# Kernel optimization log

Hardware: AMD Instinct MI355X
Metric: run time of the kernel (lower is better)

The kernel has to match this reference:

```python
import jax, jax.numpy as jnp
import numpy as np

B, N, D, H, DH, DEPTH = 4, 1024, 1024, 16, 64, 4
FI = int(D * 4.0 * 2 / 3)  # 2730, GEGLU inner dim
EPS = 1.1920929e-07  # torch float32 eps (RMSNorm default)
NEG = -jnp.finfo(jnp.float32).max


def rms(x, w):
    return x * jax.lax.rsqrt(jnp.mean(x * x, axis=-1, keepdims=True) + EPS) * w


def rope(t):
    # t: [b, h, n, d]; interleaved-pair rotary (lucidrains rotary_embedding_torch)
    n, d = t.shape[-2], t.shape[-1]
    inv_freq = 1.0 / (10000.0 ** (jnp.arange(0, d, 2, dtype=jnp.float32) / d))
    ang = jnp.arange(n, dtype=jnp.float32)[:, None] * inv_freq  # [n, d/2]
    cos = jnp.repeat(jnp.cos(ang), 2, axis=-1)  # [n, d]
    sin = jnp.repeat(jnp.sin(ang), 2, axis=-1)
    x = t.reshape(t.shape[:-1] + (d // 2, 2))
    rot = jnp.stack([-x[..., 1], x[..., 0]], axis=-1).reshape(t.shape)
    return t * cos + rot * sin


def setup_inputs() -> dict:
    key = jax.random.key(0)
    ks = jax.random.split(key, 14)
    s = 0.02
    return {
        "x": jax.random.normal(ks[0], (B, N, D), dtype=jnp.float32),
        "norm_attn_w": jnp.ones((DEPTH, D), jnp.float32),
        "wq": jax.random.normal(ks[1], (DEPTH, H * DH, D), jnp.float32) * s,
        "wkv": jax.random.normal(ks[2], (DEPTH, 2 * H * DH, D), jnp.float32) * s,
        "wo": jax.random.normal(ks[3], (DEPTH, D, H * DH), jnp.float32) * s,
        "wg": jax.random.normal(ks[4], (DEPTH, H, D), jnp.float32) * s,
        "wmix": jax.random.normal(ks[5], (DEPTH, H, D), jnp.float32) * s,
        "norm_ff_w": jnp.ones((DEPTH, D), jnp.float32),
        "ff_norm_w": jnp.ones((DEPTH, D), jnp.float32),
        "w_in": jax.random.normal(ks[6], (DEPTH, 2 * FI, D), jnp.float32) * s,
        "b_in": jnp.zeros((DEPTH, 2 * FI), jnp.float32),
        "w_out": jax.random.normal(ks[7], (DEPTH, D, FI), jnp.float32) * s,
        "b_out": jnp.zeros((DEPTH, D), jnp.float32),
        "final_norm_w": jnp.ones((D,), jnp.float32),
    }


def _forward(x, norm_attn_w, wq, wkv, wo, wg, wmix, norm_ff_w, ff_norm_w,
             w_in, b_in, w_out, b_out, final_norm_w):
    scale = DH ** -0.5
    causal = jnp.triu(jnp.ones((N, N), bool), k=1)  # True = masked
    value_residual = None
    for i in range(DEPTH):
        # --- attention block (pre-RMSNorm wrapper) ---
        h = rms(x, norm_attn_w[i])  # [b, n, d]
        q = jnp.einsum('bnd,ed->bne', h, wq[i]) * scale
        kv = jnp.einsum('bnd,ed->bne', h, wkv[i])
        k, v = jnp.split(kv, 2, axis=-1)
        split = lambda t: t.reshape(B, N, H, DH).transpose(0, 2, 1, 3)  # b h n d
        q, k, v = split(q), split(k), split(v)
        orig_v = v
        if value_residual is not None:
            mix = jax.nn.sigmoid(jnp.einsum('bnd,hd->bhn', h, wmix[i]))[..., None]
            v = v + mix * (value_residual - v)  # lerp(v, value_residual, mix)
        q, k = rope(q), rope(k)
        sim = jnp.einsum('bhid,bhjd->bhij', q, k)
        sim = jnp.where(causal, NEG, sim)
        attn = jax.nn.softmax(sim, axis=-1)
        out = jnp.einsum('bhij,bhjd->bhid', attn, v)
        gates = jax.nn.sigmoid(jnp.einsum('bnd,hd->bhn', h, wg[i]))[..., None]
        out = out * gates
        out = out.transpose(0, 2, 1, 3).reshape(B, N, H * DH)
        x = x + jnp.einsum('bne,de->bnd', out, wo[i])
        if value_residual is None:
            value_residual = orig_v
        # --- feedforward block (wrapper norm + FF's own pre-rmsnorm) ---
        g = rms(x, norm_ff_w[i])
        g = rms(g, ff_norm_w[i])
        u = jnp.einsum('bnd,ed->bne', g, w_in[i]) + b_in[i]
        a, gt = jnp.split(u, 2, axis=-1)
        u = a * jax.nn.gelu(gt, approximate=False)
        x = x + jnp.einsum('bnf,df->bnd', u, w_out[i]) + b_out[i]
    return rms(x, final_norm_w)


def reference(x, norm_attn_w, wq, wkv, wo, wg, wmix, norm_ff_w, ff_norm_w,
              w_in, b_in, w_out, b_out, final_norm_w):
    return _forward(x, norm_attn_w, wq, wkv, wo, wg, wmix, norm_ff_w,
                    ff_norm_w, w_in, b_in, w_out, b_out, final_norm_w)
```

## Files before the change

kernel.cpp:

```cpp
#include <hip/hip_runtime.h>
#include <cstdint>
#include <cstddef>


#define DEV_INLINE __device__ __forceinline__

typedef short bf16x8 __attribute__((ext_vector_type(8)));
typedef float f32x4 __attribute__((ext_vector_type(4)));

constexpr int Bsz = 4, Nseq = 1024, Dm = 1024, Hh = 16, DH = 64, NDEPTH = 4;
constexpr int FI = 2730;
constexpr int FI_PAD = 2752;
constexpr int FI_TILE = 2816;
constexpr int WIDE = 2 * FI_TILE;
constexpr int ROWS = Bsz * Nseq;
constexpr float EPSR = 1.1920929e-07f;

DEV_INLINE float bf2f(unsigned short u) {
  unsigned int x = ((unsigned int)u) << 16;
  float f; __builtin_memcpy(&f, &x, 4); return f;
}
DEV_INLINE unsigned short f2bf(float f) {
  unsigned int x; __builtin_memcpy(&x, &f, 4);
  unsigned int r = x + 0x7fffu + ((x >> 16) & 1u);
  return (unsigned short)(r >> 16);
}

using gptr_t = const __attribute__((address_space(1))) void*;
using lptr_t = __attribute__((address_space(3))) void*;
DEV_INLINE void gl_lds16(const void* g, void* l) {
  __builtin_amdgcn_global_load_lds((gptr_t)g, (lptr_t)l, 16, 0, 0);
}
DEV_INLINE void fence_mem() { asm volatile("" ::: "memory"); }

__global__ __launch_bounds__(256)
void convf2b(const float* __restrict__ src, unsigned short* __restrict__ dst,
             int src_rows, int src_cols, int dst_cols) {
  const int r = blockIdx.y;
  const int c8 = (blockIdx.x * blockDim.x + threadIdx.x) * 8;
  if (c8 >= dst_cols) return;
  alignas(16) unsigned short o[8];
  if (r < src_rows && c8 + 8 <= src_cols) {
    const float2* p = (const float2*)&src[(size_t)r * src_cols + c8];
    const float2 v0 = p[0], v1 = p[1], v2 = p[2], v3 = p[3];
    o[0] = f2bf(v0.x); o[1] = f2bf(v0.y); o[2] = f2bf(v1.x); o[3] = f2bf(v1.y);
    o[4] = f2bf(v2.x); o[5] = f2bf(v2.y); o[6] = f2bf(v3.x); o[7] = f2bf(v3.y);
  } else {
#pragma unroll
    for (int j = 0; j < 8; ++j) {
      const int c = c8 + j;
      float v = (r < src_rows && c < src_cols) ? src[(size_t)r * src_cols + c] : 0.0f;
      o[j] = f2bf(v);
    }
  }
  *(uint4*)&dst[(size_t)r * dst_cols + c8] = *(const uint4*)o;
}

__global__ __launch_bounds__(128)
void convf2b_g16(const float* __restrict__ src, unsigned short* __restrict__ dst) {
  const int p = blockIdx.y;
  const int c8 = threadIdx.x * 8;
  const int t = p >> 5, r5 = p & 31;
  const int srow = t * 16 + (r5 & 15);
  alignas(16) unsigned short o[8];
  if (srow < FI) {
    const size_t base = ((size_t)((r5 < 16) ? 0 : 1) * FI + srow) * 1024 + c8;
    const float4 v0 = *(const float4*)&src[base];
    const float4 v1 = *(const float4*)&src[base + 4];
    o[0]=f2bf(v0.x); o[1]=f2bf(v0.y); o[2]=f2bf(v0.z); o[3]=f2bf(v0.w);
    o[4]=f2bf(v1.x); o[5]=f2bf(v1.y); o[6]=f2bf(v1.z); o[7]=f2bf(v1.w);
  } else {
#pragma unroll
    for (int j = 0; j < 8; ++j) o[j] = 0;
  }
  *(uint4*)&dst[(size_t)p * 1024 + c8] = *(const uint4*)o;
}

__global__ __launch_bounds__(256)
void rope_tables(float* __restrict__ cost, float* __restrict__ sint) {
  int idx = blockIdx.x * 256 + threadIdx.x;
  if (idx >= Nseq * 32) return;
  int n = idx >> 5, p = idx & 31;
  float freq = powf(10000.0f, -(float)(2 * p) * (1.0f / 64.0f));
  float ang = (float)n * freq;
  cost[idx] = cosf(ang);
  sint[idx] = sinf(ang);
}

__global__ __launch_bounds__(256)
void rms_one(const float* __restrict__ x, const float* __restrict__ w,
             unsigned short* __restrict__ out) {
  __shared__ float sred[4];
  const int row = blockIdx.x, tid = threadIdx.x;
  const float4 v = ((const float4*)(x + (size_t)row * Dm))[tid];
  float ss = v.x * v.x + v.y * v.y + v.z * v.z + v.w * v.w;
#pragma unroll
  for (int o = 32; o >= 1; o >>= 1) ss += __shfl_xor(ss, o, 64);
  if ((tid & 63) == 0) sred[tid >> 6] = ss;
  __syncthreads();
  float rs = rsqrtf((sred[0] + sred[1] + sred[2] + sred[3]) * (1.0f / Dm) + EPSR);
  const float4 wv = ((const float4*)w)[tid];
  alignas(8) unsigned short o4[4] = { f2bf(v.x * rs * wv.x), f2bf(v.y * rs * wv.y),
                                      f2bf(v.z * rs * wv.z), f2bf(v.w * rs * wv.w) };
  *(uint2*)&out[(size_t)row * Dm + tid * 4] = *(const uint2*)o4;
}

__global__ __launch_bounds__(256)
void rms_ff(const float* __restrict__ x, const float* __restrict__ w1,
            const float* __restrict__ w2, unsigned short* __restrict__ out) {
  __shared__ float sred[4];
  const int row = blockIdx.x, tid = threadIdx.x;
  const float4 v = ((const float4*)(x + (size_t)row * Dm))[tid];
  const float4 w1v = ((const float4*)w1)[tid];
  const float4 w2v = ((const float4*)w2)[tid];
  float ss = v.x * v.x + v.y * v.y + v.z * v.z + v.w * v.w;
#pragma unroll
  for (int o = 32; o >= 1; o >>= 1) ss += __shfl_xor(ss, o, 64);
  if ((tid & 63) == 0) sred[tid >> 6] = ss;
  __syncthreads();
  float rs1 = rsqrtf((sred[0] + sred[1] + sred[2] + sred[3]) * (1.0f / Dm) + EPSR);
  float t0 = v.x * rs1 * w1v.x, t1 = v.y * rs1 * w1v.y;
  float t2 = v.z * rs1 * w1v.z, t3 = v.w * rs1 * w1v.w;
  float ss2 = t0 * t0 + t1 * t1 + t2 * t2 + t3 * t3;
#pragma unroll
  for (int o = 32; o >= 1; o >>= 1) ss2 += __shfl_xor(ss2, o, 64);
  __syncthreads();
  if ((tid & 63) == 0) sred[tid >> 6] = ss2;
  __syncthreads();
  float rs2 = rsqrtf((sred[0] + sred[1] + sred[2] + sred[3]) * (1.0f / Dm) + EPSR);
  alignas(8) unsigned short o4[4] = { f2bf(t0 * rs2 * w2v.x), f2bf(t1 * rs2 * w2v.y),
                                      f2bf(t2 * rs2 * w2v.z), f2bf(t3 * rs2 * w2v.w) };
  *(uint2*)&out[(size_t)row * Dm + tid * 4] = *(const uint2*)o4;
}

__global__ __launch_bounds__(256)
void rms_final(const float* __restrict__ x, const float* __restrict__ w,
               float* __restrict__ out) {
  __shared__ float sred[4];
  const int row = blockIdx.x, tid = threadIdx.x;
  const float4 v = ((const float4*)(x + (size_t)row * Dm))[tid];
  float ss = v.x * v.x + v.y * v.y + v.z * v.z + v.w * v.w;
#pragma unroll
  for (int o = 32; o >= 1; o >>= 1) ss += __shfl_xor(ss, o, 64);
  if ((tid & 63) == 0) sred[tid >> 6] = ss;
  __syncthreads();
  float rs = rsqrtf((sred[0] + sred[1] + sred[2] + sred[3]) * (1.0f / Dm) + EPSR);
  const float4 wv = ((const float4*)w)[tid];
  float4 o;
  o.x = v.x * rs * wv.x; o.y = v.y * rs * wv.y;
  o.z = v.z * rs * wv.z; o.w = v.w * rs * wv.w;
  ((float4*)(out + (size_t)row * Dm))[tid] = o;
}

template <int MODE>
__global__ __launch_bounds__(256)
void gemm_nt(const unsigned short* __restrict__ A,
             const unsigned short* __restrict__ Bw,
             void* __restrict__ Cout,
             const float* __restrict__ bias,
             const float* __restrict__ resid,
             int K, int ldc, int n_store) {
  __shared__ unsigned short As[2][128 * 64];
  __shared__ unsigned short Bs[2][128 * 64];
  const int tid = threadIdx.x;
  const int m0 = blockIdx.x * 128;
  const int n0 = blockIdx.y * 128;
  const int w = tid >> 6, l = tid & 63;
  const int wm = (w >> 1) * 64, wn = (w & 1) * 64;
  const int lr = l & 15, lg = l >> 4;
  const int lsub = l & 7, lrow8 = l >> 3;
  const int colsw = (lsub ^ lrow8) << 3;
  const unsigned short* gA = &A[(size_t)(m0 + w * 8 + lrow8) * K + colsw];
  const unsigned short* gB = &Bw[(size_t)(n0 + w * 8 + lrow8) * K + colsw];
  const size_t rstep = (size_t)32 * K;
  f32x4 acc[4][4] = {};

  auto stage = [&](int buf, int kt) {
    const int o = kt * 64;
#pragma unroll
    for (int i = 0; i < 4; ++i) {
      gl_lds16(gA + i * rstep + o, &As[buf][i * 2048 + w * 512]);
      gl_lds16(gB + i * rstep + o, &Bs[buf][i * 2048 + w * 512]);
    }
  };
  auto compute = [&](int buf) {
    bf16x8 af[2][4], bfr[2][4];
#pragma unroll
    for (int ks = 0; ks < 2; ++ks) {
      const int slot = (ks * 4 + lg) ^ (lr & 7);
#pragma unroll
      for (int fj = 0; fj < 4; ++fj)
        bfr[ks][fj] = *(const bf16x8*)&Bs[buf][(wn + fj * 16 + lr) * 64 + slot * 8];
#pragma unroll
      for (int fi = 0; fi < 4; ++fi)
        af[ks][fi] = *(const bf16x8*)&As[buf][(wm + fi * 16 + lr) * 64 + slot * 8];
    }
    __builtin_amdgcn_s_setprio(1);
#pragma unroll
    for (int ks = 0; ks < 2; ++ks)
#pragma unroll
      for (int fi = 0; fi < 4; ++fi)
#pragma unroll
        for (int fj = 0; fj < 4; ++fj)
          acc[fi][fj] = __builtin_amdgcn_mfma_f32_16x16x32_bf16(af[ks][fi], bfr[ks][fj], acc[fi][fj], 0, 0, 0);
    __builtin_amdgcn_s_setprio(0);
  };

  const int nk = K >> 6;
  stage(0, 0);
  asm volatile("s_waitcnt vmcnt(0)" ::: "memory");
  __builtin_amdgcn_s_barrier();
  fence_mem();
  int cur = 0;
#pragma unroll 1
  for (int kt = 0; kt < nk; ++kt) {
    const bool more = (kt + 1 < nk);
    if (more) stage(cur ^ 1, kt + 1);
    compute(cur);
    if (more) {
      asm volatile("s_waitcnt vmcnt(0)" ::: "memory");
      __builtin_amdgcn_s_barrier();
      fence_mem();
    }
    cur ^= 1;
  }

#pragma unroll
  for (int fi = 0; fi < 4; ++fi) {
    const int rowb = m0 + wm + fi * 16 + lg * 4;
#pragma unroll
    for (int fj = 0; fj < 4; ++fj) {
      const int col = n0 + wn + fj * 16 + lr;
#pragma unroll
      for (int r = 0; r < 4; ++r) {
        const float val = acc[fi][fj][r];
        const int rr = rowb + r;
        if constexpr (MODE == 1) {
          if (col < n_store)
            ((float*)Cout)[(size_t)rr * ldc + col] = 1.0f / (1.0f + __expf(-val));
        } else {
          const float bv = bias ? bias[col] : 0.0f;
          ((float*)Cout)[(size_t)rr * ldc + col] =
              resid[(size_t)rr * ldc + col] + val + bv;
        }
      }
    }
  }
}

template <int MODE>
__global__ __launch_bounds__(512, 2)
void gemm_nt256(const unsigned short* __restrict__ A,
                const unsigned short* __restrict__ Bw,
                void* __restrict__ Cout,
                const float* __restrict__ bias,
                int K, int ldc, int nm, int nn) {
  __shared__ unsigned short As[2][256 * 64];
  __shared__ unsigned short Bs[2][256 * 64];
  const int tid = threadIdx.x;
  const int nwg = nm * nn;
  const int qq = nwg >> 3;
  const int xcd = blockIdx.x & 7, orig = blockIdx.x >> 3;
  const int wgid = xcd * qq + orig;
  const int m0 = (wgid % nm) * 256;
  const int n0 = (wgid / nm) * 256;
  const int w = tid >> 6, l = tid & 63;
  const int wm = (w >> 2) * 128, wn = (w & 3) * 64;
  const int lr = l & 15, lg = l >> 4;
  const int lsub = l & 7, lrow8 = l >> 3;
  const int colsw = (lsub ^ lrow8) << 3;
  const unsigned short* gA = &A[(size_t)(m0 + w * 8 + lrow8) * K + colsw];
  const unsigned short* gB = &Bw[(size_t)(n0 + w * 8 + lrow8) * K + colsw];
  const size_t rstep = (size_t)64 * K;
  f32x4 acc[8][4] = {};

  auto stage_part = [&](int buf, int kt, int part) {
    const int o = kt * 64;
    const int i0 = (part & 1) * 2;
    if (part < 2) {
      gl_lds16(gA + (size_t)i0 * rstep + o,       &As[buf][i0 * 4096 + w * 512]);
      gl_lds16(gA + (size_t)(i0 + 1) * rstep + o, &As[buf][(i0 + 1) * 4096 + w * 512]);
    } else {
      gl_lds16(gB + (size_t)i0 * rstep + o,       &Bs[buf][i0 * 4096 + w * 512]);
      gl_lds16(gB + (size_t)(i0 + 1) * rstep + o, &Bs[buf][(i0 + 1) * 4096 + w * 512]);
    }
  };

  const int nk = K >> 6;
  stage_part(0, 0, 0); stage_part(0, 0, 1);
  stage_part(0, 0, 2); stage_part(0, 0, 3);
  asm volatile("s_waitcnt vmcnt(0)" ::: "memory");
  __builtin_amdgcn_s_barrier();
  fence_mem();

#pragma unroll 1
  for (int t = 0; t < nk; ++t) {
    const int p = t & 1;
    const bool more = (t + 1 < nk);
    bf16x8 bfr[4];
#pragma unroll
    for (int q = 0; q < 4; ++q) {
      const int ks = q >> 1, half = q & 1;
      const int slot = (ks * 4 + lg) ^ (lr & 7);
      if (half == 0) {
#pragma unroll
        for (int fj = 0; fj < 4; ++fj)
          bfr[fj] = *(const bf16x8*)&Bs[p][(wn + fj * 16 + lr) * 64 + slot * 8];
      }
      bf16x8 af[4];
#pragma unroll
      for (int fi = 0; fi < 4; ++fi)
        af[fi] = *(const bf16x8*)&As[p][(wm + half * 64 + fi * 16 + lr) * 64 + slot * 8];
      if (more) stage_part(p ^ 1, t + 1, q);
      __builtin_amdgcn_s_setprio(1);
#pragma unroll
      for (int fi = 0; fi < 4; ++fi)
#pragma unroll
        for (int fj = 0; fj < 4; ++fj)
          acc[half * 4 + fi][fj] =
              __builtin_amdgcn_mfma_f32_16x16x32_bf16(af[fi], bfr[fj], acc[half * 4 + fi][fj], 0, 0, 0);
      __builtin_amdgcn_s_setprio(0);
      if (q < 3) {
        __builtin_amdgcn_s_barrier();
        fence_mem();
      }
    }
    if (more) {
      asm volatile("s_waitcnt vmcnt(0)" ::: "memory");
      __builtin_amdgcn_s_barrier();
      fence_mem();
    }
  }

#pragma unroll
  for (int fi = 0; fi < 8; ++fi) {
    const int rowb = m0 + wm + fi * 16 + lg * 4;
    if constexpr (MODE == 0) {
#pragma unroll
      for (int fj = 0; fj < 4; ++fj) {
        const int col = n0 + wn + fj * 16 + lr;
#pragma unroll
        for (int r = 0; r < 4; ++r)
          ((unsigned short*)Cout)[(size_t)(rowb + r) * ldc + col] = f2bf(acc[fi][fj][r]);
      }
    } else {
#pragma unroll
      for (int fjp = 0; fjp < 2; ++fjp) {
        const int ucol = ((n0 + wn) >> 1) + fjp * 16 + lr;
        if (ucol >= FI_PAD) continue;
        const bool live = (ucol < FI);
        const float ba = live ? bias[ucol] : 0.0f;
        const float bg = live ? bias[FI + ucol] : 0.0f;
#pragma unroll
        for (int r = 0; r < 4; ++r) {
          const float va = acc[fi][2 * fjp][r] + ba;
          const float vg = acc[fi][2 * fjp + 1][r] + bg;
          const float gel = 0.5f * vg * (1.0f + erff(vg * 0.70710678118654752f));
          ((unsigned short*)Cout)[(size_t)(rowb + r) * ldc + ucol] =
              f2bf(live ? va * gel : 0.0f);
        }
      }
    }
  }
}

__global__ __launch_bounds__(256)
void rope_qk(const unsigned short* __restrict__ qkv_lin,
             const float* __restrict__ cost, const float* __restrict__ sint,
             unsigned short* __restrict__ qb, unsigned short* __restrict__ kb) {
  const int nt = blockIdx.x, bh = blockIdx.y;
  const int b = bh >> 4, h = bh & 15;
  const int tid = threadIdx.x;
  const int pi = tid & 31, r0 = tid >> 5;
  const float scale = 0.125f;
#pragma unroll
  for (int j = 0; j < 8; ++j) {
    const int n = nt * 64 + r0 + j * 8;
    const int nf = b * Nseq + n;
    const float c = cost[n * 32 + pi], s = sint[n * 32 + pi];
    const unsigned short* qp = &qkv_lin[(size_t)nf * 3072 + h * 64 + pi * 2];
    float q0 = bf2f(qp[0]), q1 = bf2f(qp[1]);
    alignas(4) unsigned short oq[2];
    oq[0] = f2bf((q0 * c - q1 * s) * scale);
    oq[1] = f2bf((q1 * c + q0 * s) * scale);
    *(unsigned int*)&qb[((size_t)bh * Nseq + n) * 64 + pi * 2] = *(const unsigned int*)oq;
    const unsigned short* kp = &qkv_lin[(size_t)nf * 3072 + 1024 + h * 64 + pi * 2];
    float k0 = bf2f(kp[0]), k1 = bf2f(kp[1]);
    alignas(4) unsigned short ok[2];
    ok[0] = f2bf(k0 * c - k1 * s);
    ok[1] = f2bf(k1 * c + k0 * s);
    *(unsigned int*)&kb[((size_t)bh * Nseq + n) * 64 + pi * 2] = *(const unsigned int*)ok;
  }
}

__global__ __launch_bounds__(256)
void v_mix_pack(const unsigned short* __restrict__ qkv_lin,
                const float* __restrict__ gm,
                unsigned short* __restrict__ vres,
                unsigned short* __restrict__ vtb, int layer) {
  __shared__ unsigned short T[64][72];
  const int nt = blockIdx.x, bh = blockIdx.y;
  const int b = bh >> 4, h = bh & 15;
  const int tid = threadIdx.x;
#pragma unroll
  for (int p = 0; p < 2; ++p) {
    int c = tid + p * 256;
    int nl = c >> 3, cg = (c & 7) << 3;
    int n = nt * 64 + nl, nf = b * Nseq + n;
    uint4 vv = *(const uint4*)&qkv_lin[(size_t)nf * 3072 + 2048 + h * 64 + cg];
    if (layer == 0) {
      *(uint4*)&vres[((size_t)bh * Nseq + n) * 64 + cg] = vv;
      *(uint4*)&T[nl][cg] = vv;
    } else {
      alignas(16) unsigned short ve[8]; *(uint4*)ve = vv;
      uint4 rv = *(const uint4*)&vres[((size_t)bh * Nseq + n) * 64 + cg];
      alignas(16) unsigned short re[8]; *(uint4*)re = rv;
      const float mix = gm[(size_t)nf * 32 + 16 + h];
      alignas(16) unsigned short oe[8];
#pragma unroll
      for (int j = 0; j < 8; ++j) {
        float v = bf2f(ve[j]), rr = bf2f(re[j]);
        oe[j] = f2bf(v + mix * (rr - v));
      }
      *(uint4*)&T[nl][cg] = *(const uint4*)oe;
    }
  }
  __syncthreads();
#pragma unroll
  for (int p = 0; p < 2; ++p) {
    int c = tid + p * 256;
    int d = c >> 3, ng = (c & 7) << 3;
    alignas(16) unsigned short oe[8];
#pragma unroll
    for (int j = 0; j < 8; ++j) oe[j] = T[ng + j][d];
    *(uint4*)&vtb[(size_t)bh * 65536 + (size_t)d * Nseq + nt * 64 + ng] = *(const uint4*)oe;
  }
}

__global__ __launch_bounds__(256)
void attn_fwd(const unsigned short* __restrict__ qb,
              const unsigned short* __restrict__ kb,
              const unsigned short* __restrict__ vtb,
              const float* __restrict__ gm,
              unsigned short* __restrict__ attn_out) {
  __shared__ unsigned short Ps[4][16][72];
  const int bid = blockIdx.x;
  const int x = bid & 7, rest = bid >> 3;
  const int bh = x * 8 + (rest & 7);
  const int qt = 15 - (rest >> 3);
  const int b = bh >> 4, h = bh & 15;
  const int tid = threadIdx.x;
  const int w = tid >> 6, l = tid & 63;
  const int lr = l & 15, lg = l >> 4;
  const int q0 = qt * 64 + w * 16;
  const size_t head = (size_t)bh * Nseq * DH;

  bf16x8 aq[2];
  aq[0] = *(const bf16x8*)&qb[head + (size_t)(q0 + lr) * DH + lg * 8];
  aq[1] = *(const bf16x8*)&qb[head + (size_t)(q0 + lr) * DH + 32 + lg * 8];

  float mrow[4] = {-1e30f, -1e30f, -1e30f, -1e30f};
  float lsum[4] = {0.f, 0.f, 0.f, 0.f};
  f32x4 acco[4] = {};

  for (int kt = 0; kt <= qt; ++kt) {
    const int kv0 = kt * 64;
    f32x4 s[4];
#pragma unroll
    for (int t = 0; t < 4; ++t) {
      bf16x8 bk0 = *(const bf16x8*)&kb[head + (size_t)(kv0 + t * 16 + lr) * DH + lg * 8];
      bf16x8 bk1 = *(const bf16x8*)&kb[head + (size_t)(kv0 + t * 16 + lr) * DH + 32 + lg * 8];
      f32x4 z = {};
      z = __builtin_amdgcn_mfma_f32_16x16x32_bf16(aq[0], bk0, z, 0, 0, 0);
      z = __builtin_amdgcn_mfma_f32_16x16x32_bf16(aq[1], bk1, z, 0, 0, 0);
      s[t] = z;
    }
    const bool diag = (kt == qt);
    float mx4[4];
    bool need = false;
#pragma unroll
    for (int r = 0; r < 4; ++r) {
      const int qr = q0 + lg * 4 + r;
      float mx = -1e30f;
#pragma unroll
      for (int t = 0; t < 4; ++t) {
        float sv = s[t][r];
        if (diag && (kv0 + t * 16 + lr > qr)) sv = -1e30f;
        s[t][r] = sv;
        mx = fmaxf(mx, sv);
      }
      mx = fmaxf(mx, __shfl_xor(mx, 1, 64));
      mx = fmaxf(mx, __shfl_xor(mx, 2, 64));
      mx = fmaxf(mx, __shfl_xor(mx, 4, 64));
      mx = fmaxf(mx, __shfl_xor(mx, 8, 64));
      mx4[r] = mx;
      need = need || (mx > mrow[r] + 8.0f);
    }
    if (__any(need)) {
#pragma unroll
      for (int r = 0; r < 4; ++r) {
        const float mn = fmaxf(mrow[r], mx4[r]);
        const float alpha = __expf(mrow[r] - mn);
        mrow[r] = mn;
        lsum[r] *= alpha;
#pragma unroll
        for (int dt = 0; dt < 4; ++dt) acco[dt][r] *= alpha;
      }
    }
#pragma unroll
    for (int r = 0; r < 4; ++r) {
      float rs = 0.f;
#pragma unroll
      for (int t = 0; t < 4; ++t) {
        float pv = __expf(s[t][r] - mrow[r]);
        s[t][r] = pv;
        rs += pv;
      }
      rs += __shfl_xor(rs, 1, 64);
      rs += __shfl_xor(rs, 2, 64);
      rs += __shfl_xor(rs, 4, 64);
      rs += __shfl_xor(rs, 8, 64);
      lsum[r] += rs;
    }
#pragma unroll
    for (int t = 0; t < 4; ++t)
#pragma unroll
      for (int r = 0; r < 4; ++r)
        Ps[w][lg * 4 + r][t * 16 + lr] = f2bf(s[t][r]);
#pragma unroll
    for (int ks = 0; ks < 2; ++ks) {
      bf16x8 ap = *(const bf16x8*)&Ps[w][lr][ks * 32 + lg * 8];
#pragma unroll
      for (int dt = 0; dt < 4; ++dt) {
        bf16x8 bv = *(const bf16x8*)&vtb[head + (size_t)(dt * 16 + lr) * Nseq + kv0 + ks * 32 + lg * 8];
        acco[dt] = __builtin_amdgcn_mfma_f32_16x16x32_bf16(ap, bv, acco[dt], 0, 0, 0);
      }
    }
  }
#pragma unroll
  for (int r = 0; r < 4; ++r) {
    const int qr = q0 + lg * 4 + r;
    const int nf = b * Nseq + qr;
    const float gate = gm[(size_t)nf * 32 + h];
    const float inv = 1.0f / lsum[r];
#pragma unroll
    for (int dt = 0; dt < 4; ++dt)
      attn_out[(size_t)nf * Dm + h * DH + dt * 16 + lr] = f2bf(acco[dt][r] * inv * gate);
  }
}

extern "C" void kernel_launch(void* const* d_in, const int* in_sizes, int n_in,
                              void* d_out, int out_size, void* d_ws, size_t ws_size,
                              hipStream_t stream) {
  const float* x_in  = (const float*)d_in[0];
  const float* naw   = (const float*)d_in[1];
  const float* wq    = (const float*)d_in[2];
  const float* wkv   = (const float*)d_in[3];
  const float* wo    = (const float*)d_in[4];
  const float* wg    = (const float*)d_in[5];
  const float* wmix  = (const float*)d_in[6];
  const float* nfw   = (const float*)d_in[7];
  const float* ffw   = (const float*)d_in[8];
  const float* w_in  = (const float*)d_in[9];
  const float* b_in  = (const float*)d_in[10];
  const float* w_out = (const float*)d_in[11];
  const float* b_out = (const float*)d_in[12];
  const float* fnw   = (const float*)d_in[13];

  uint8_t* ws = (uint8_t*)d_ws;
  size_t off = 0;
  auto alloc = [&](size_t bytes) -> void* {
    void* p = ws + off;
    off += (bytes + 255) & ~(size_t)255;
    return p;
  };
  float*          x_res    = (float*)alloc((size_t)ROWS * Dm * 4);
  unsigned short* h        = (unsigned short*)alloc((size_t)ROWS * Dm * 2);
  unsigned short* qkv_lin  = (unsigned short*)alloc((size_t)ROWS * 3072 * 2);
  float*          gm       = (float*)alloc((size_t)ROWS * 32 * 4);
  unsigned short* qb       = (unsigned short*)alloc((size_t)64 * Nseq * DH * 2);
  unsigned short* kb       = (unsigned short*)alloc((size_t)64 * Nseq * DH * 2);
  unsigned short* vtb      = (unsigned short*)alloc((size_t)64 * Nseq * DH * 2);
  unsigned short* vres     = (unsigned short*)alloc((size_t)64 * Nseq * DH * 2);
  unsigned short* attn     = (unsigned short*)alloc((size_t)ROWS * Dm * 2);
  float*          cost     = (float*)alloc((size_t)Nseq * 32 * 4);
  float*          sint     = (float*)alloc((size_t)Nseq * 32 * 4);
  unsigned short* wqkv_bf  = (unsigned short*)alloc((size_t)3072 * 1024 * 2);
  unsigned short* wo_bf    = (unsigned short*)alloc((size_t)1024 * 1024 * 2);
  unsigned short* wgm_bf   = (unsigned short*)alloc((size_t)128 * 1024 * 2);
  unsigned short* win_bf   = (unsigned short*)alloc((size_t)WIDE * 1024 * 2);
  unsigned short* wout_bf  = (unsigned short*)alloc((size_t)1024 * FI_PAD * 2);
  unsigned short* u = qkv_lin;

  hipMemcpyAsync(x_res, x_in, (size_t)ROWS * Dm * 4, hipMemcpyDeviceToDevice, stream);
  rope_tables<<<128, 256, 0, stream>>>(cost, sint);

  for (int i = 0; i < NDEPTH; ++i) {
    convf2b<<<dim3(1, 1024), 128, 0, stream>>>(wq + (size_t)i * 1024 * 1024, wqkv_bf, 1024, 1024, 1024);
    convf2b<<<dim3(1, 2048), 128, 0, stream>>>(wkv + (size_t)i * 2048 * 1024, wqkv_bf + (size_t)1024 * 1024, 2048, 1024, 1024);
    convf2b<<<dim3(1, 1024), 128, 0, stream>>>(wo + (size_t)i * 1024 * 1024, wo_bf, 1024, 1024, 1024);
    convf2b<<<dim3(1, 16), 128, 0, stream>>>(wg + (size_t)i * 16 * 1024, wgm_bf, 16, 1024, 1024);
    convf2b<<<dim3(1, 16), 128, 0, stream>>>(wmix + (size_t)i * 16 * 1024, wgm_bf + 16 * 1024, 16, 1024, 1024);
    convf2b<<<dim3(1, 96), 128, 0, stream>>>(wg, wgm_bf + 32 * 1024, 0, 1024, 1024);
    convf2b_g16<<<dim3(1, WIDE), 128, 0, stream>>>(w_in + (size_t)i * 2 * FI * 1024, win_bf);
    convf2b<<<dim3(2, 1024), 256, 0, stream>>>(w_out + (size_t)i * 1024 * FI, wout_bf, 1024, FI, FI_PAD);

    rms_one<<<ROWS, 256, 0, stream>>>(x_res, naw + i * 1024, h);
    gemm_nt256<0><<<192, 512, 0, stream>>>(h, wqkv_bf, qkv_lin, nullptr, 1024, 3072, 16, 12);
    gemm_nt<1><<<dim3(32, 1), 256, 0, stream>>>(h, wgm_bf, gm, nullptr, nullptr, 1024, 32, 32);
    rope_qk<<<dim3(16, 64), 256, 0, stream>>>(qkv_lin, cost, sint, qb, kb);
    v_mix_pack<<<dim3(16, 64), 256, 0, stream>>>(qkv_lin, gm, vres, vtb, i);
    attn_fwd<<<1024, 256, 0, stream>>>(qb, kb, vtb, gm, attn);
    gemm_nt<2><<<dim3(32, 8), 256, 0, stream>>>(attn, wo_bf, x_res, nullptr, x_res, 1024, 1024, 1024);
    rms_ff<<<ROWS, 256, 0, stream>>>(x_res, nfw + i * 1024, ffw + i * 1024, h);
    gemm_nt256<3><<<352, 512, 0, stream>>>(h, win_bf, u, b_in + (size_t)i * 2 * FI, 1024, FI_PAD, 16, 22);
    gemm_nt<2><<<dim3(32, 8), 256, 0, stream>>>(u, wout_bf, x_res, b_out + i * 1024, x_res, FI_PAD, 1024, 1024);
  }
  rms_final<<<ROWS, 256, 0, stream>>>(x_res, fnw, (float*)d_out);
}
```

Measured before the change: 1.520 ms.

## Issue GEMM tile prefetch upfront and double-buffer K loads in attention

```diff
diff --git a/kernel.cpp b/kernel.cpp
--- a/kernel.cpp
+++ b/kernel.cpp
@@ -274,21 +274,18 @@
   const size_t rstep = (size_t)64 * K;
   f32x4 acc[8][4] = {};
 
-  auto stage_part = [&](int buf, int kt, int part) {
+  auto stage_all = [&](int buf, int kt) {
     const int o = kt * 64;
-    const int i0 = (part & 1) * 2;
-    if (part < 2) {
-      gl_lds16(gA + (size_t)i0 * rstep + o,       &As[buf][i0 * 4096 + w * 512]);
-      gl_lds16(gA + (size_t)(i0 + 1) * rstep + o, &As[buf][(i0 + 1) * 4096 + w * 512]);
-    } else {
-      gl_lds16(gB + (size_t)i0 * rstep + o,       &Bs[buf][i0 * 4096 + w * 512]);
-      gl_lds16(gB + (size_t)(i0 + 1) * rstep + o, &Bs[buf][(i0 + 1) * 4096 + w * 512]);
-    }
+#pragma unroll
+    for (int i = 0; i < 4; ++i)
+      gl_lds16(gA + (size_t)i * rstep + o, &As[buf][i * 4096 + w * 512]);
+#pragma unroll
+    for (int i = 0; i < 4; ++i)
+      gl_lds16(gB + (size_t)i * rstep + o, &Bs[buf][i * 4096 + w * 512]);
   };
 
   const int nk = K >> 6;
-  stage_part(0, 0, 0); stage_part(0, 0, 1);
-  stage_part(0, 0, 2); stage_part(0, 0, 3);
+  stage_all(0, 0);
   asm volatile("s_waitcnt vmcnt(0)" ::: "memory");
   __builtin_amdgcn_s_barrier();
   fence_mem();
@@ -297,6 +294,7 @@
   for (int t = 0; t < nk; ++t) {
     const int p = t & 1;
     const bool more = (t + 1 < nk);
+    if (more) stage_all(p ^ 1, t + 1);
     bf16x8 bfr[4];
 #pragma unroll
     for (int q = 0; q < 4; ++q) {
@@ -311,7 +309,6 @@
 #pragma unroll
       for (int fi = 0; fi < 4; ++fi)
         af[fi] = *(const bf16x8*)&As[p][(wm + half * 64 + fi * 16 + lr) * 64 + slot * 8];
-      if (more) stage_part(p ^ 1, t + 1, q);
       __builtin_amdgcn_s_setprio(1);
 #pragma unroll
       for (int fi = 0; fi < 4; ++fi)
@@ -463,16 +460,22 @@
   float lsum[4] = {0.f, 0.f, 0.f, 0.f};
   f32x4 acco[4] = {};
 
-  for (int kt = 0; kt <= qt; ++kt) {
+  auto loadK = [&](bf16x8 (&kf)[8], int kv0) {
+#pragma unroll
+    for (int t = 0; t < 4; ++t) {
+      kf[2 * t]     = *(const bf16x8*)&kb[head + (size_t)(kv0 + t * 16 + lr) * DH + lg * 8];
+      kf[2 * t + 1] = *(const bf16x8*)&kb[head + (size_t)(kv0 + t * 16 + lr) * DH + 32 + lg * 8];
+    }
+  };
+
+  auto process = [&](int kt, const bf16x8 (&kf)[8]) {
     const int kv0 = kt * 64;
     f32x4 s[4];
 #pragma unroll
     for (int t = 0; t < 4; ++t) {
-      bf16x8 bk0 = *(const bf16x8*)&kb[head + (size_t)(kv0 + t * 16 + lr) * DH + lg * 8];
-      bf16x8 bk1 = *(const bf16x8*)&kb[head + (size_t)(kv0 + t * 16 + lr) * DH + 32 + lg * 8];
       f32x4 z = {};
-      z = __builtin_amdgcn_mfma_f32_16x16x32_bf16(aq[0], bk0, z, 0, 0, 0);
-      z = __builtin_amdgcn_mfma_f32_16x16x32_bf16(aq[1], bk1, z, 0, 0, 0);
+      z = __builtin_amdgcn_mfma_f32_16x16x32_bf16(aq[0], kf[2 * t], z, 0, 0, 0);
+      z = __builtin_amdgcn_mfma_f32_16x16x32_bf16(aq[1], kf[2 * t + 1], z, 0, 0, 0);
       s[t] = z;
     }
     const bool diag = (kt == qt);
@@ -536,7 +539,19 @@
         acco[dt] = __builtin_amdgcn_mfma_f32_16x16x32_bf16(ap, bv, acco[dt], 0, 0, 0);
       }
     }
-  }
+  };
+
+  bf16x8 kfA[8], kfB[8];
+  loadK(kfA, 0);
+  for (int kt = 0; kt <= qt; kt += 2) {
+    if (kt < qt) loadK(kfB, (kt + 1) * 64);
+    process(kt, kfA);
+    if (kt + 1 <= qt) {
+      if (kt + 1 < qt) loadK(kfA, (kt + 2) * 64);
+      process(kt + 1, kfB);
+    }
+  }
+
 #pragma unroll
   for (int r = 0; r < 4; ++r) {
     const int qr = q0 + lg * 4 + r;
```

Measured after the change: 1.553 ms. 1.02x slower.

## Prefetch GEMM tiles two stages ahead with split A/B staging and partial waits

Applied to the files above, without the earlier changes.

```diff
diff --git a/kernel.cpp b/kernel.cpp
--- a/kernel.cpp
+++ b/kernel.cpp
@@ -175,54 +175,70 @@
   const size_t rstep = (size_t)32 * K;
   f32x4 acc[4][4] = {};
 
-  auto stage = [&](int buf, int kt) {
+  auto stage_A = [&](int buf, int kt) {
     const int o = kt * 64;
 #pragma unroll
-    for (int i = 0; i < 4; ++i) {
+    for (int i = 0; i < 4; ++i)
       gl_lds16(gA + i * rstep + o, &As[buf][i * 2048 + w * 512]);
+  };
+  auto stage_B = [&](int buf, int kt) {
+    const int o = kt * 64;
+#pragma unroll
+    for (int i = 0; i < 4; ++i)
       gl_lds16(gB + i * rstep + o, &Bs[buf][i * 2048 + w * 512]);
-    }
   };
-  auto compute = [&](int buf) {
-    bf16x8 af[2][4], bfr[2][4];
+
+  const int nk = K >> 6;
+  stage_B(0, 0); stage_A(0, 0);
+  if (nk > 1) { stage_B(1, 1); stage_A(1, 1); }
+  if (nk > 1) asm volatile("s_waitcnt vmcnt(8)" ::: "memory");
+  else        asm volatile("s_waitcnt vmcnt(0)" ::: "memory");
+  __builtin_amdgcn_s_barrier();
+  fence_mem();
+
+#pragma unroll 1
+  for (int t = 0; t < nk; ++t) {
+    const int p = t & 1;
+    bf16x8 bfr[2][4];
 #pragma unroll
     for (int ks = 0; ks < 2; ++ks) {
       const int slot = (ks * 4 + lg) ^ (lr & 7);
 #pragma unroll
       for (int fj = 0; fj < 4; ++fj)
-        bfr[ks][fj] = *(const bf16x8*)&Bs[buf][(wn + fj * 16 + lr) * 64 + slot * 8];
-#pragma unroll
-      for (int fi = 0; fi < 4; ++fi)
-        af[ks][fi] = *(const bf16x8*)&As[buf][(wm + fi * 16 + lr) * 64 + slot * 8];
-    }
-    __builtin_amdgcn_s_setprio(1);
-#pragma unroll
-    for (int ks = 0; ks < 2; ++ks)
-#pragma unroll
-      for (int fi = 0; fi < 4; ++fi)
+        bfr[ks][fj] = *(const bf16x8*)&Bs[p][(wn + fj * 16 + lr) * 64 + slot * 8];
+    }
+#pragma unroll
+    for (int q = 0; q < 4; ++q) {
+      bf16x8 af[2];
+#pragma unroll
+      for (int ks = 0; ks < 2; ++ks) {
+        const int slot = (ks * 4 + lg) ^ (lr & 7);
+        af[ks] = *(const bf16x8*)&As[p][(wm + q * 16 + lr) * 64 + slot * 8];
+      }
+      __builtin_amdgcn_s_setprio(1);
+#pragma unroll
+      for (int ks = 0; ks < 2; ++ks)
 #pragma unroll
         for (int fj = 0; fj < 4; ++fj)
-          acc[fi][fj] = __builtin_amdgcn_mfma_f32_16x16x32_bf16(af[ks][fi], bfr[ks][fj], acc[fi][fj], 0, 0, 0);
-    __builtin_amdgcn_s_setprio(0);
-  };
-
-  const int nk = K >> 6;
-  stage(0, 0);
-  asm volatile("s_waitcnt vmcnt(0)" ::: "memory");
-  __builtin_amdgcn_s_barrier();
-  fence_mem();
-  int cur = 0;
-#pragma unroll 1
-  for (int kt = 0; kt < nk; ++kt) {
-    const bool more = (kt + 1 < nk);
-    if (more) stage(cur ^ 1, kt + 1);
-    compute(cur);
-    if (more) {
-      asm volatile("s_waitcnt vmcnt(0)" ::: "memory");
+          acc[q][fj] = __builtin_amdgcn_mfma_f32_16x16x32_bf16(af[ks], bfr[ks][fj], acc[q][fj], 0, 0, 0);
+      __builtin_amdgcn_s_setprio(0);
+      if (q == 0) {
+        fence_mem();
+        __builtin_amdgcn_s_barrier();
+        fence_mem();
+        if (t + 2 < nk) stage_B(p, t + 2);
+      }
+    }
+    fence_mem();
+    __builtin_amdgcn_s_barrier();
+    fence_mem();
+    if (t + 2 < nk) stage_A(p, t + 2);
+    if (t + 1 < nk) {
+      if (t + 2 < nk) asm volatile("s_waitcnt vmcnt(8)" ::: "memory");
+      else            asm volatile("s_waitcnt vmcnt(0)" ::: "memory");
       __builtin_amdgcn_s_barrier();
       fence_mem();
     }
-    cur ^= 1;
   }
 
 #pragma unroll
@@ -274,59 +290,71 @@
   const size_t rstep = (size_t)64 * K;
   f32x4 acc[8][4] = {};
 
-  auto stage_part = [&](int buf, int kt, int part) {
+  auto stage_A = [&](int buf, int kt) {
     const int o = kt * 64;
-    const int i0 = (part & 1) * 2;
-    if (part < 2) {
-      gl_lds16(gA + (size_t)i0 * rstep + o,       &As[buf][i0 * 4096 + w * 512]);
-      gl_lds16(gA + (size_t)(i0 + 1) * rstep + o, &As[buf][(i0 + 1) * 4096 + w * 512]);
-    } else {
-      gl_lds16(gB + (size_t)i0 * rstep + o,       &Bs[buf][i0 * 4096 + w * 512]);
-      gl_lds16(gB + (size_t)(i0 + 1) * rstep + o, &Bs[buf][(i0 + 1) * 4096 + w * 512]);
-    }
+#pragma unroll
+    for (int i = 0; i < 4; ++i)
+      gl_lds16(gA + (size_t)i * rstep + o, &As[buf][i * 4096 + w * 512]);
   };
+  auto stage_B = [&](int buf, int kt) {
+    const int o = kt * 64;
+#pragma unroll
+    for (int i = 0; i < 4; ++i)
+      gl_lds16(gB + (size_t)i * rstep + o, &Bs[buf][i * 4096 + w * 512]);
+  };
 
   const int nk = K >> 6;
-  stage_part(0, 0, 0); stage_part(0, 0, 1);
-  stage_part(0, 0, 2); stage_part(0, 0, 3);
-  asm volatile("s_waitcnt vmcnt(0)" ::: "memory");
+  stage_B(0, 0); stage_A(0, 0);
+  if (nk > 1) { stage_B(1, 1); stage_A(1, 1); }
+  if (nk > 1) asm volatile("s_waitcnt vmcnt(8)" ::: "memory");
+  else        asm volatile("s_waitcnt vmcnt(0)" ::: "memory");
   __builtin_amdgcn_s_barrier();
   fence_mem();
 
 #pragma unroll 1
   for (int t = 0; t < nk; ++t) {
     const int p = t & 1;
-    const bool more = (t + 1 < nk);
-    bf16x8 bfr[4];
+    bf16x8 bfr[2][4];
+#pragma unroll
+    for (int ks = 0; ks < 2; ++ks) {
+      const int slot = (ks * 4 + lg) ^ (lr & 7);
+#pragma unroll
+      for (int fj = 0; fj < 4; ++fj)
+        bfr[ks][fj] = *(const bf16x8*)&Bs[p][(wn + fj * 16 + lr) * 64 + slot * 8];
+    }
 #pragma unroll
     for (int q = 0; q < 4; ++q) {
-      const int ks = q >> 1, half = q & 1;
-      const int slot = (ks * 4 + lg) ^ (lr & 7);
-      if (half == 0) {
-#pragma unroll
-        for (int fj = 0; fj < 4; ++fj)
-          bfr[fj] = *(const bf16x8*)&Bs[p][(wn + fj * 16 + lr) * 64 + slot * 8];
-      }
-      bf16x8 af[4];
-#pragma unroll
-      for (int fi = 0; fi < 4; ++fi)
-        af[fi] = *(const bf16x8*)&As[p][(wm + half * 64 + fi * 16 + lr) * 64 + slot * 8];
-      if (more) stage_part(p ^ 1, t + 1, q);
+      bf16x8 af[2][2];
+#pragma unroll
+      for (int ks = 0; ks < 2; ++ks) {
+        const int slot = (ks * 4 + lg) ^ (lr & 7);
+        af[ks][0] = *(const bf16x8*)&As[p][(wm + (2 * q) * 16 + lr) * 64 + slot * 8];
+        af[ks][1] = *(const bf16x8*)&As[p][(wm + (2 * q + 1) * 16 + lr) * 64 + slot * 8];
+      }
       __builtin_amdgcn_s_setprio(1);
 #pragma unroll
-      for (int fi = 0; fi < 4; ++fi)
-#pragma unroll
-        for (int fj = 0; fj < 4; ++fj)
-          acc[half * 4 + fi][fj] =
-              __builtin_amdgcn_mfma_f32_16x16x32_bf16(af[fi], bfr[fj], acc[half * 4 + fi][fj], 0, 0, 0);
+      for (int ks = 0; ks < 2; ++ks)
+#pragma unroll
+        for (int i = 0; i < 2; ++i)
+#pragma unroll
+          for (int fj = 0; fj < 4; ++fj)
+            acc[2 * q + i][fj] = __builtin_amdgcn_mfma_f32_16x16x32_bf16(
+                af[ks][i], bfr[ks][fj], acc[2 * q + i][fj], 0, 0, 0);
       __builtin_amdgcn_s_setprio(0);
-      if (q < 3) {
+      if (q == 0) {
+        fence_mem();
         __builtin_amdgcn_s_barrier();
         fence_mem();
-      }
-    }
-    if (more) {
-      asm volatile("s_waitcnt vmcnt(0)" ::: "memory");
+        if (t + 2 < nk) stage_B(p, t + 2);
+      }
+    }
+    fence_mem();
+    __builtin_amdgcn_s_barrier();
+    fence_mem();
+    if (t + 2 < nk) stage_A(p, t + 2);
+    if (t + 1 < nk) {
+      if (t + 2 < nk) asm volatile("s_waitcnt vmcnt(8)" ::: "memory");
+      else            asm volatile("s_waitcnt vmcnt(0)" ::: "memory");
       __builtin_amdgcn_s_barrier();
       fence_mem();
     }
```

New measurement: 1.536 ms. Within noise of the previous version (+1.1%).

## Double-buffer K and V tiles in LDS with async global-to-LDS loads

Applied to the files above, without the earlier changes.

```diff
diff --git a/kernel.cpp b/kernel.cpp
--- a/kernel.cpp
+++ b/kernel.cpp
@@ -443,6 +443,8 @@
               const unsigned short* __restrict__ vtb,
               const float* __restrict__ gm,
               unsigned short* __restrict__ attn_out) {
+  __shared__ unsigned short Ks[2][64 * 64];
+  __shared__ unsigned short Vs[2][64 * 64];
   __shared__ unsigned short Ps[4][16][72];
   const int bid = blockIdx.x;
   const int x = bid & 7, rest = bid >> 3;
@@ -454,6 +456,20 @@
   const int lr = l & 15, lg = l >> 4;
   const int q0 = qt * 64 + w * 16;
   const size_t head = (size_t)bh * Nseq * DH;
+  const int lrow8 = l >> 3;
+  const int colsw = ((l & 7) ^ lrow8) << 3;
+
+  auto stageKV = [&](int buf, int kt) {
+    const int kv0 = kt * 64;
+#pragma unroll
+    for (int i = 0; i < 2; ++i) {
+      const int rb = w * 16 + i * 8;
+      gl_lds16(&kb[head + (size_t)(kv0 + rb + lrow8) * DH + colsw],
+               &Ks[buf][rb * 64]);
+      gl_lds16(&vtb[head + (size_t)(rb + lrow8) * Nseq + kv0 + colsw],
+               &Vs[buf][rb * 64]);
+    }
+  };
 
   bf16x8 aq[2];
   aq[0] = *(const bf16x8*)&qb[head + (size_t)(q0 + lr) * DH + lg * 8];
@@ -463,13 +479,23 @@
   float lsum[4] = {0.f, 0.f, 0.f, 0.f};
   f32x4 acco[4] = {};
 
+  stageKV(0, 0);
+  asm volatile("s_waitcnt vmcnt(0)" ::: "memory");
+  __builtin_amdgcn_s_barrier();
+  fence_mem();
+
+#pragma unroll 1
   for (int kt = 0; kt <= qt; ++kt) {
+    const int p = kt & 1;
     const int kv0 = kt * 64;
+    const bool more = (kt < qt);
+    if (more) stageKV(p ^ 1, kt + 1);
     f32x4 s[4];
 #pragma unroll
     for (int t = 0; t < 4; ++t) {
-      bf16x8 bk0 = *(const bf16x8*)&kb[head + (size_t)(kv0 + t * 16 + lr) * DH + lg * 8];
-      bf16x8 bk1 = *(const bf16x8*)&kb[head + (size_t)(kv0 + t * 16 + lr) * DH + 32 + lg * 8];
+      const int krow = t * 16 + lr;
+      bf16x8 bk0 = *(const bf16x8*)&Ks[p][krow * 64 + ((0 + lg) ^ (lr & 7)) * 8];
+      bf16x8 bk1 = *(const bf16x8*)&Ks[p][krow * 64 + ((4 + lg) ^ (lr & 7)) * 8];
       f32x4 z = {};
       z = __builtin_amdgcn_mfma_f32_16x16x32_bf16(aq[0], bk0, z, 0, 0, 0);
       z = __builtin_amdgcn_mfma_f32_16x16x32_bf16(aq[1], bk1, z, 0, 0, 0);
@@ -532,11 +558,18 @@
       bf16x8 ap = *(const bf16x8*)&Ps[w][lr][ks * 32 + lg * 8];
 #pragma unroll
       for (int dt = 0; dt < 4; ++dt) {
-        bf16x8 bv = *(const bf16x8*)&vtb[head + (size_t)(dt * 16 + lr) * Nseq + kv0 + ks * 32 + lg * 8];
+        const int vrow = dt * 16 + lr;
+        bf16x8 bv = *(const bf16x8*)&Vs[p][vrow * 64 + ((ks * 4 + lg) ^ (lr & 7)) * 8];
         acco[dt] = __builtin_amdgcn_mfma_f32_16x16x32_bf16(ap, bv, acco[dt], 0, 0, 0);
       }
     }
-  }
+    if (more) {
+      asm volatile("s_waitcnt vmcnt(0)" ::: "memory");
+      __builtin_amdgcn_s_barrier();
+      fence_mem();
+    }
+  }
+
 #pragma unroll
   for (int r = 0; r < 4; ++r) {
     const int qr = q0 + lg * 4 + r;
```

New measurement: 1.338 ms. 11.9% less time.
